# Kernel tuning notes

Hardware: AMD Instinct MI355X
Metric: run time of the kernel (lower is better)

The kernel has to match this reference:

```python
import jax, jax.numpy as jnp
import numpy as np

NEIGHBOR_RATE = 0.1  # neighbor_rate init arg
LEAKY_SLOPE = 0.2
NEG_INF = -1.0e9


def setup_inputs() -> dict:
    key = jax.random.key(0)
    k1, k2, k3, k4 = jax.random.split(key, 4)
    B, N, Din, H, hd = 4, 2048, 128, 4, 32  # output_dim = H*hd = 128
    h = jax.random.normal(k1, (B, N, Din), jnp.float32)
    adj = jax.random.uniform(k2, (B, N, N), jnp.float32)
    # stacked per-head params: W[k] in [Din, hd], a[k] in [2*hd]
    w_bound = 1.0 / np.sqrt(Din)
    a_bound = 1.0 / np.sqrt(2 * hd)
    W = jax.random.uniform(k3, (H, Din, hd), jnp.float32, -w_bound, w_bound)
    a = jax.random.uniform(k4, (H, 2 * hd), jnp.float32, -a_bound, a_bound)
    return {"h": h, "adj": adj, "W": W, "a": a}


def reference(h, adj, W, a):
    B, N, _ = h.shape
    H, _, hd = W.shape
    k = int(NEIGHBOR_RATE * N)  # num_neighbors
    # Wh: [B,H,N,hd]
    Wh = jnp.einsum('bnf,hfd->bhnd', h, W)
    # cat([Wh_i, Wh_j]) @ a  ==  Wh_i @ a[:hd] + Wh_j @ a[hd:] (broadcast trick)
    s_i = jnp.einsum('bhnd,hd->bhn', Wh, a[:, :hd])
    s_j = jnp.einsum('bhnd,hd->bhn', Wh, a[:, hd:])
    e = jax.nn.leaky_relu(s_i[..., :, None] + s_j[..., None, :], LEAKY_SLOPE)  # [B,H,N,N]
    # top-k mask along last (neighbor) axis, built by scatter like torch .scatter_
    _, idx = jax.lax.top_k(e, k)  # [B,H,N,k]
    row_mask = lambda i: jnp.zeros((N,), jnp.bool_).at[i].set(True)
    mask = jax.vmap(row_mask)(idx.reshape(-1, k)).reshape(e.shape)
    masked = jnp.where(mask, e, NEG_INF)
    attn = jax.nn.softmax(masked, axis=-1) * adj[:, None]  # [B,H,N,N]
    hp = jnp.einsum('bhnm,bhmd->bhnd', attn, Wh)
    # concat heads on feature dim -> [B,N,H*hd]
    return hp.transpose(0, 2, 1, 3).reshape(B, N, H * hd)
```

## Files before the change

kernel.cpp:

```cpp
#include <hip/hip_runtime.h>
#include <hip/hip_bf16.h>
#include <cmath>

#define BB 4
#define NN 2048
#define DIN 128
#define HH 4
#define HD 32
#define KSEL 204
#define BH (BB*HH)
#define KPAD 256
#define KST 264

typedef __attribute__((ext_vector_type(8))) short short8;
typedef __attribute__((ext_vector_type(4))) short short4v;
typedef __attribute__((ext_vector_type(4))) float float4v;

static __device__ inline short f2bf(float x) {
    __hip_bfloat16 b = __float2bfloat16(x);
    return __builtin_bit_cast(short, b);
}

__global__ __launch_bounds__(256) void s_kernel(const float* __restrict__ h,
                                                const float* __restrict__ W,
                                                const float* __restrict__ a,
                                                float* __restrict__ si, float* __restrict__ sj) {
    int bh = blockIdx.x >> 3, chunk = blockIdx.x & 7;
    int b = bh >> 2, hh = bh & 3;
    __shared__ float w1[128], w2[128];
    int t = threadIdx.x;
    {
        int f = t & 127, half = t >> 7;
        const float* Wp = W + (size_t)hh * (DIN * HD) + f * HD;
        const float* ap = a + hh * 64 + half * 32;
        float acc = 0.f;
#pragma unroll
        for (int d = 0; d < 32; ++d) acc += Wp[d] * ap[d];
        if (half == 0) w1[f] = acc; else w2[f] = acc;
    }
    __syncthreads();
    int n = chunk * 256 + t;
    const float4* hr = (const float4*)(h + ((size_t)b * NN + n) * DIN);
    float s1 = 0.f, s2 = 0.f;
#pragma unroll 8
    for (int q = 0; q < 32; ++q) {
        float4 x = hr[q];
        s1 += x.x * w1[q*4] + x.y * w1[q*4+1] + x.z * w1[q*4+2] + x.w * w1[q*4+3];
        s2 += x.x * w2[q*4] + x.y * w2[q*4+1] + x.z * w2[q*4+2] + x.w * w2[q*4+3];
    }
    int o = bh * NN + n;
    si[o] = s1; sj[o] = s2;
}

__global__ __launch_bounds__(1024) void select_kernel(
        const float* __restrict__ h, const float* __restrict__ W,
        const float* __restrict__ sj,
        int* __restrict__ idxsel, float* __restrict__ sjsel,
        float* __restrict__ sjmax, short* __restrict__ Whsel) {
    int bh = blockIdx.x;
    int b = bh >> 2, hh = bh & 3;
    int t = threadIdx.x, lane = t & 63, w = t >> 6;
    __shared__ float sv[NN];
    __shared__ short WT[32][136];
    __shared__ int hist16[16][256];
    __shared__ int binInfo[2];
    __shared__ int wtot[4];
    __shared__ int wtotg[16], wtote[16], woffg[16], woffe[16];
    __shared__ float wmax[16];
    __shared__ int idxLDS[KSEL];

    for (int e = t; e < 32 * 128; e += 1024) {
        int n = e >> 7, k = e & 127;
        WT[n][k] = f2bf(W[(size_t)hh * (DIN * HD) + k * HD + n]);
    }

    const float* s = sj + (size_t)bh * NN;
    int j0 = t * 2;
    float2 xx = *(const float2*)(s + j0);
    sv[j0] = xx.x; sv[j0 + 1] = xx.y;
    unsigned u0 = __builtin_bit_cast(unsigned, xx.x);
    unsigned u1 = __builtin_bit_cast(unsigned, xx.y);
    u0 = (u0 & 0x80000000u) ? ~u0 : (u0 | 0x80000000u);
    u1 = (u1 & 0x80000000u) ? ~u1 : (u1 | 0x80000000u);
    float lmax = fmaxf(xx.x, xx.y);
#pragma unroll
    for (int off = 32; off >= 1; off >>= 1) lmax = fmaxf(lmax, __shfl_xor(lmax, off));
    if (lane == 0) wmax[w] = lmax;
    __syncthreads();
    if (t == 0) {
        float m = wmax[0];
#pragma unroll
        for (int i = 1; i < 16; ++i) m = fmaxf(m, wmax[i]);
        sjmax[bh] = m;
    }

    unsigned prefix = 0;
    int need = KSEL;
#pragma unroll
    for (int shift = 24; shift >= 0; shift -= 8) {
        ((int*)hist16)[t] = 0; ((int*)hist16)[t + 1024] = 0;
        ((int*)hist16)[t + 2048] = 0; ((int*)hist16)[t + 3072] = 0;
        __syncthreads();
        unsigned hmask = (shift < 24) ? (0xFFFFFFFFu << (shift + 8)) : 0u;
        if (((u0 ^ prefix) & hmask) == 0) atomicAdd(&hist16[w][(u0 >> shift) & 255], 1);
        if (((u1 ^ prefix) & hmask) == 0) atomicAdd(&hist16[w][(u1 >> shift) & 255], 1);
        __syncthreads();
        int sc = 0, hv = 0, bb = 0;
        if (t < 256) {
            bb = 255 - t;
            hv = 0;
#pragma unroll
            for (int i = 0; i < 16; ++i) hv += hist16[i][bb];
            sc = hv;
#pragma unroll
            for (int off = 1; off < 64; off <<= 1) {
                int u = __shfl_up(sc, off);
                if (lane >= off) sc += u;
            }
            if (lane == 63) wtot[w] = sc;
        }
        __syncthreads();
        if (t < 256) {
            int woffset = 0;
#pragma unroll
            for (int i = 0; i < 4; ++i) woffset += (i < w) ? wtot[i] : 0;
            int incl = sc + woffset;
            int excl = incl - hv;
            if (incl >= need && excl < need) {
                binInfo[0] = bb;
                binInfo[1] = excl;
            }
        }
        __syncthreads();
        prefix |= ((unsigned)binInfo[0]) << shift;
        need -= binInfo[1];
        __syncthreads();
    }
    unsigned T = prefix;
    int n_gt = KSEL - need;

    int cg = (u0 > T ? 1 : 0) + (u1 > T ? 1 : 0);
    int ce = (u0 == T ? 1 : 0) + (u1 == T ? 1 : 0);
    int sg = cg, se = ce;
#pragma unroll
    for (int off = 1; off < 64; off <<= 1) {
        int ug = __shfl_up(sg, off), ue = __shfl_up(se, off);
        if (lane >= off) { sg += ug; se += ue; }
    }
    if (lane == 63) { wtotg[w] = sg; wtote[w] = se; }
    __syncthreads();
    if (t == 0) {
        int rg = 0, re = 0;
#pragma unroll
        for (int i = 0; i < 16; ++i) {
            woffg[i] = rg; rg += wtotg[i];
            woffe[i] = re; re += wtote[i];
        }
    }
    __syncthreads();
    int pg = woffg[w] + sg - cg;
    int te = woffe[w] + se - ce;
    {
        unsigned kk[2] = {u0, u1};
#pragma unroll
        for (int r = 0; r < 2; ++r) {
            int j = j0 + r;
            if (kk[r] > T) {
                idxsel[bh * KSEL + pg] = j;
                sjsel[bh * KSEL + pg] = sv[j];
                idxLDS[pg] = j;
                pg++;
            } else if (kk[r] == T) {
                if (te < need) {
                    int pos = n_gt + te;
                    idxsel[bh * KSEL + pos] = j;
                    sjsel[bh * KSEL + pos] = sv[j];
                    idxLDS[pos] = j;
                }
                te++;
            }
        }
    }
    __syncthreads();

    {
        int mr = lane & 15, quad = lane >> 4;
        int jjp = w * 16 + mr;
        bool valid = jjp < KSEL;
        const float* hrow = h + ((size_t)b * NN + (valid ? idxLDS[jjp] : 0)) * DIN + quad * 8;
        float4v acc0 = {0.f, 0.f, 0.f, 0.f};
        float4v acc1 = {0.f, 0.f, 0.f, 0.f};
#pragma unroll
        for (int ks = 0; ks < 4; ++ks) {
            short8 afr;
            if (valid) {
                float4 xa = *(const float4*)(hrow + ks * 32);
                float4 xb = *(const float4*)(hrow + ks * 32 + 4);
                afr[0] = f2bf(xa.x); afr[1] = f2bf(xa.y); afr[2] = f2bf(xa.z); afr[3] = f2bf(xa.w);
                afr[4] = f2bf(xb.x); afr[5] = f2bf(xb.y); afr[6] = f2bf(xb.z); afr[7] = f2bf(xb.w);
            } else {
                afr = (short8){0, 0, 0, 0, 0, 0, 0, 0};
            }
            short8 b0 = *(const short8*)&WT[mr][ks * 32 + quad * 8];
            short8 b1 = *(const short8*)&WT[16 + mr][ks * 32 + quad * 8];
            acc0 = __builtin_amdgcn_mfma_f32_16x16x32_bf16(afr, b0, acc0, 0, 0, 0);
            acc1 = __builtin_amdgcn_mfma_f32_16x16x32_bf16(afr, b1, acc1, 0, 0, 0);
        }
        short4v o0, o1;
#pragma unroll
        for (int r = 0; r < 4; ++r) { o0[r] = f2bf(acc0[r]); o1[r] = f2bf(acc1[r]); }
        size_t base = (size_t)bh * HD * KPAD;
        int jjs = w * 16 + quad * 4;
        *(short4v*)&Whsel[base + (size_t)mr * KPAD + jjs] = o0;
        *(short4v*)&Whsel[base + (size_t)(16 + mr) * KPAD + jjs] = o1;
    }
}

__global__ __launch_bounds__(256) void attn2_kernel(
        const float* __restrict__ adj, const float* __restrict__ si,
        const int* __restrict__ idxsel, const float* __restrict__ sjsel,
        const float* __restrict__ sjmax, const short* __restrict__ Whsel,
        float* __restrict__ out) {
    int b = blockIdx.x >> 7;
    int tile = blockIdx.x & 127;
    __shared__ float adjbuf[4][NN];
    __shared__ short PSb[HH][16][KST];
    __shared__ int   idxS[HH][KPAD];
    __shared__ float sjS[HH][KPAD];
    __shared__ float invZS[HH][16];
    __shared__ float smaxS[HH];
    int t = threadIdx.x, w = t >> 6, lane = t & 63;
    int mr = lane & 15, quad = lane >> 4;

    for (int e = t; e < HH * KPAD; e += 256) {
        int hh = e >> 8, jj = e & 255;
        bool v = jj < KSEL;
        idxS[hh][jj] = v ? idxsel[(b * HH + hh) * KSEL + jj] : 0;
        sjS[hh][jj]  = v ? sjsel[(b * HH + hh) * KSEL + jj] : -1e30f;
    }
    if (t < HH) smaxS[t] = sjmax[b * HH + t];

    short8 bfr[2][8];
    {
        const short* wp = Whsel + (size_t)((b * HH + w) * HD) * KPAD;
#pragma unroll
        for (int ni = 0; ni < 2; ++ni)
#pragma unroll
            for (int ks = 0; ks < 8; ++ks)
                bfr[ni][ks] = *(const short8*)(wp + (size_t)(ni * 16 + mr) * KPAD + ks * 32 + quad * 8);
    }

    int i0 = tile * 16;
    const float* adjb = adj + (size_t)b * NN * NN;
    {
        const float4* src = (const float4*)(adjb + (size_t)i0 * NN);
        float4* dst = (float4*)adjbuf;
#pragma unroll
        for (int q = 0; q < 8; ++q)
            dst[q * 256 + t] = src[q * 256 + t];
    }
    __syncthreads();

    int bh = b * HH + w;
    float smax = smaxS[w];
    for (int s = 0; s < 4; ++s) {
#pragma unroll
        for (int r = 0; r < 4; ++r) {
            int i_loc = s * 4 + r;
            int i = i0 + i_loc;
            float siv = si[(size_t)bh * NN + i];
            float m = siv + smax;
            m = (m >= 0.f) ? m : 0.2f * m;
            float z = 0.f;
            short* prow = &PSb[w][i_loc][0];
#pragma unroll
            for (int k = 0; k < 2; ++k) {
                int jj = k * 128 + lane * 2;
                int ja = idxS[w][jj], jb = idxS[w][jj + 1];
                float ava = adjbuf[r][ja], avb = adjbuf[r][jb];
                float ea = siv + sjS[w][jj];
                float eb = siv + sjS[w][jj + 1];
                ea = (ea >= 0.f) ? ea : 0.2f * ea;
                eb = (eb >= 0.f) ? eb : 0.2f * eb;
                float ca = __expf(ea - m);
                float cb = __expf(eb - m);
                z += ca + cb;
                short2 p;
                p.x = f2bf(ca * ava);
                p.y = f2bf(cb * avb);
                *(short2*)&prow[jj] = p;
            }
#pragma unroll
            for (int off = 32; off >= 1; off >>= 1) z += __shfl_xor(z, off);
            if (lane == 0) invZS[w][i_loc] = 1.0f / z;
        }
        if (s < 3) {
            __syncthreads();
            const float4* src = (const float4*)(adjb + (size_t)(i0 + (s + 1) * 4) * NN);
            float4* dst = (float4*)adjbuf;
#pragma unroll
            for (int q = 0; q < 8; ++q)
                dst[q * 256 + t] = src[q * 256 + t];
            __syncthreads();
        }
    }
#pragma unroll
    for (int ni = 0; ni < 2; ++ni) {
        float4v acc = {0.f, 0.f, 0.f, 0.f};
#pragma unroll
        for (int ks = 0; ks < 8; ++ks) {
            short8 afr = *(const short8*)&PSb[w][mr][ks * 32 + quad * 8];
            acc = __builtin_amdgcn_mfma_f32_16x16x32_bf16(afr, bfr[ni][ks], acc, 0, 0, 0);
        }
#pragma unroll
        for (int r = 0; r < 4; ++r) {
            int i_loc = quad * 4 + r;
            int d = ni * 16 + mr;
            out[((size_t)(b * NN + i0 + i_loc)) * (HH * HD) + w * HD + d] =
                acc[r] * invZS[w][i_loc];
        }
    }
}

extern "C" void kernel_launch(void* const* d_in, const int* in_sizes, int n_in,
                              void* d_out, int out_size, void* d_ws, size_t ws_size,
                              hipStream_t stream) {
    const float* h   = (const float*)d_in[0];
    const float* adj = (const float*)d_in[1];
    const float* W   = (const float*)d_in[2];
    const float* a   = (const float*)d_in[3];
    float* out = (float*)d_out;

    float* si     = (float*)d_ws;
    float* sj     = si + (size_t)BH * NN;
    float* sjsel  = sj + (size_t)BH * NN;
    float* sjmax  = sjsel + (size_t)BH * KSEL;
    int*   idxsel = (int*)(sjmax + 16);
    short* Whsel  = (short*)(idxsel + (size_t)BH * KSEL);

    s_kernel<<<BH * 8, 256, 0, stream>>>(h, W, a, si, sj);
    select_kernel<<<BH, 1024, 0, stream>>>(h, W, sj, idxsel, sjsel, sjmax, Whsel);
    attn2_kernel<<<BB * 128, 256, 0, stream>>>(adj, si, idxsel, sjsel, sjmax, Whsel, out);
}
```

Baseline: 127.9 us.

## Double-buffer adj rows via register prefetch and compute all heads per row in s_kernel

The attention kernel now stages adj in two-row chunks with a double-buffered LDS array, prefetching the next chunk into registers while the current rows are processed. This removes one barrier per step and hides global-load latency. The score kernel now has 4 threads share each h row and compute all 4 heads' dot products, reducing them with shuffles. This reads h once instead of once per head, but each block recomputes all heads' projected a-vectors.

```diff
diff --git a/kernel.cpp b/kernel.cpp
--- a/kernel.cpp
+++ b/kernel.cpp
@@ -25,31 +25,56 @@
                                                 const float* __restrict__ W,
                                                 const float* __restrict__ a,
                                                 float* __restrict__ si, float* __restrict__ sj) {
-    int bh = blockIdx.x >> 3, chunk = blockIdx.x & 7;
-    int b = bh >> 2, hh = bh & 3;
-    __shared__ float w1[128], w2[128];
+    __shared__ float w1L[HH][DIN], w2L[HH][DIN];
     int t = threadIdx.x;
-    {
-        int f = t & 127, half = t >> 7;
-        const float* Wp = W + (size_t)hh * (DIN * HD) + f * HD;
+    for (int e = t; e < 8 * DIN; e += 256) {
+        int f = e & 127, v = e >> 7;
+        int hh = v >> 1, half = v & 1;
+        const float* Wp = W + ((size_t)hh * DIN + f) * HD;
         const float* ap = a + hh * 64 + half * 32;
         float acc = 0.f;
 #pragma unroll
         for (int d = 0; d < 32; ++d) acc += Wp[d] * ap[d];
-        if (half == 0) w1[f] = acc; else w2[f] = acc;
-    }
-    __syncthreads();
-    int n = chunk * 256 + t;
-    const float4* hr = (const float4*)(h + ((size_t)b * NN + n) * DIN);
-    float s1 = 0.f, s2 = 0.f;
-#pragma unroll 8
-    for (int q = 0; q < 32; ++q) {
-        float4 x = hr[q];
-        s1 += x.x * w1[q*4] + x.y * w1[q*4+1] + x.z * w1[q*4+2] + x.w * w1[q*4+3];
-        s2 += x.x * w2[q*4] + x.y * w2[q*4+1] + x.z * w2[q*4+2] + x.w * w2[q*4+3];
-    }
-    int o = bh * NN + n;
-    si[o] = s1; sj[o] = s2;
+        if (half == 0) w1L[hh][f] = acc; else w2L[hh][f] = acc;
+    }
+    __syncthreads();
+
+    int gid = blockIdx.x * 256 + t;
+    int row = gid >> 2;
+    int q   = gid & 3;
+    int b = row >> 11, n = row & 2047;
+    const float* hr = h + (size_t)row * DIN;
+
+    float s1h0 = 0.f, s1h1 = 0.f, s1h2 = 0.f, s1h3 = 0.f;
+    float s2h0 = 0.f, s2h1 = 0.f, s2h2 = 0.f, s2h3 = 0.f;
+#pragma unroll
+    for (int i = 0; i < 8; ++i) {
+        int f = q * 4 + i * 16;
+        float4 x = *(const float4*)(hr + f);
+        const float* wa0 = &w1L[0][f]; const float* wb0 = &w2L[0][f];
+        const float* wa1 = &w1L[1][f]; const float* wb1 = &w2L[1][f];
+        const float* wa2 = &w1L[2][f]; const float* wb2 = &w2L[2][f];
+        const float* wa3 = &w1L[3][f]; const float* wb3 = &w2L[3][f];
+        s1h0 += x.x*wa0[0] + x.y*wa0[1] + x.z*wa0[2] + x.w*wa0[3];
+        s2h0 += x.x*wb0[0] + x.y*wb0[1] + x.z*wb0[2] + x.w*wb0[3];
+        s1h1 += x.x*wa1[0] + x.y*wa1[1] + x.z*wa1[2] + x.w*wa1[3];
+        s2h1 += x.x*wb1[0] + x.y*wb1[1] + x.z*wb1[2] + x.w*wb1[3];
+        s1h2 += x.x*wa2[0] + x.y*wa2[1] + x.z*wa2[2] + x.w*wa2[3];
+        s2h2 += x.x*wb2[0] + x.y*wb2[1] + x.z*wb2[2] + x.w*wb2[3];
+        s1h3 += x.x*wa3[0] + x.y*wa3[1] + x.z*wa3[2] + x.w*wa3[3];
+        s2h3 += x.x*wb3[0] + x.y*wb3[1] + x.z*wb3[2] + x.w*wb3[3];
+    }
+#pragma unroll
+    for (int off = 1; off <= 2; off <<= 1) {
+        s1h0 += __shfl_xor(s1h0, off); s2h0 += __shfl_xor(s2h0, off);
+        s1h1 += __shfl_xor(s1h1, off); s2h1 += __shfl_xor(s2h1, off);
+        s1h2 += __shfl_xor(s1h2, off); s2h2 += __shfl_xor(s2h2, off);
+        s1h3 += __shfl_xor(s1h3, off); s2h3 += __shfl_xor(s2h3, off);
+    }
+    float o1 = (q == 0) ? s1h0 : (q == 1) ? s1h1 : (q == 2) ? s1h2 : s1h3;
+    float o2 = (q == 0) ? s2h0 : (q == 1) ? s2h1 : (q == 2) ? s2h2 : s2h3;
+    size_t o = (size_t)(b * HH + q) * NN + n;
+    si[o] = o1; sj[o] = o2;
 }
 
 __global__ __launch_bounds__(1024) void select_kernel(
@@ -223,7 +248,7 @@
         float* __restrict__ out) {
     int b = blockIdx.x >> 7;
     int tile = blockIdx.x & 127;
-    __shared__ float adjbuf[4][NN];
+    __shared__ float adjbuf[2][2][NN];
     __shared__ short PSb[HH][16][KST];
     __shared__ int   idxS[HH][KPAD];
     __shared__ float sjS[HH][KPAD];
@@ -232,6 +257,16 @@
     int t = threadIdx.x, w = t >> 6, lane = t & 63;
     int mr = lane & 15, quad = lane >> 4;
 
+    int i0 = tile * 16;
+    const float* adjb = adj + (size_t)b * NN * NN + (size_t)i0 * NN;
+
+    float4 pre[4];
+    {
+        const float4* src = (const float4*)adjb;
+#pragma unroll
+        for (int q = 0; q < 4; ++q) pre[q] = src[q * 256 + t];
+    }
+
     for (int e = t; e < HH * KPAD; e += 256) {
         int hh = e >> 8, jj = e & 255;
         bool v = jj < KSEL;
@@ -250,25 +285,25 @@
                 bfr[ni][ks] = *(const short8*)(wp + (size_t)(ni * 16 + mr) * KPAD + ks * 32 + quad * 8);
     }
 
-    int i0 = tile * 16;
-    const float* adjb = adj + (size_t)b * NN * NN;
-    {
-        const float4* src = (const float4*)(adjb + (size_t)i0 * NN);
-        float4* dst = (float4*)adjbuf;
-#pragma unroll
-        for (int q = 0; q < 8; ++q)
-            dst[q * 256 + t] = src[q * 256 + t];
+    {
+        float4* dst = (float4*)(&adjbuf[0][0][0]);
+#pragma unroll
+        for (int q = 0; q < 4; ++q) dst[q * 256 + t] = pre[q];
     }
     __syncthreads();
 
     int bh = b * HH + w;
     float smax = smaxS[w];
-    for (int s = 0; s < 4; ++s) {
-#pragma unroll
-        for (int r = 0; r < 4; ++r) {
-            int i_loc = s * 4 + r;
-            int i = i0 + i_loc;
-            float siv = si[(size_t)bh * NN + i];
+    for (int s = 0; s < 8; ++s) {
+        if (s < 7) {
+            const float4* src = (const float4*)(adjb + (size_t)(s + 1) * 2 * NN);
+#pragma unroll
+            for (int q = 0; q < 4; ++q) pre[q] = src[q * 256 + t];
+        }
+#pragma unroll
+        for (int r = 0; r < 2; ++r) {
+            int i_loc = s * 2 + r;
+            float siv = si[(size_t)bh * NN + i0 + i_loc];
             float m = siv + smax;
             m = (m >= 0.f) ? m : 0.2f * m;
             float z = 0.f;
@@ -277,7 +312,7 @@
             for (int k = 0; k < 2; ++k) {
                 int jj = k * 128 + lane * 2;
                 int ja = idxS[w][jj], jb = idxS[w][jj + 1];
-                float ava = adjbuf[r][ja], avb = adjbuf[r][jb];
+                float ava = adjbuf[s & 1][r][ja], avb = adjbuf[s & 1][r][jb];
                 float ea = siv + sjS[w][jj];
                 float eb = siv + sjS[w][jj + 1];
                 ea = (ea >= 0.f) ? ea : 0.2f * ea;
@@ -294,15 +329,12 @@
             for (int off = 32; off >= 1; off >>= 1) z += __shfl_xor(z, off);
             if (lane == 0) invZS[w][i_loc] = 1.0f / z;
         }
-        if (s < 3) {
-            __syncthreads();
-            const float4* src = (const float4*)(adjb + (size_t)(i0 + (s + 1) * 4) * NN);
-            float4* dst = (float4*)adjbuf;
-#pragma unroll
-            for (int q = 0; q < 8; ++q)
-                dst[q * 256 + t] = src[q * 256 + t];
-            __syncthreads();
-        }
+        if (s < 7) {
+            float4* dst = (float4*)(&adjbuf[(s + 1) & 1][0][0]);
+#pragma unroll
+            for (int q = 0; q < 4; ++q) dst[q * 256 + t] = pre[q];
+        }
+        __syncthreads();
     }
 #pragma unroll
     for (int ni = 0; ni < 2; ++ni) {
@@ -338,7 +370,7 @@
     int*   idxsel = (int*)(sjmax + 16);
     short* Whsel  = (short*)(idxsel + (size_t)BH * KSEL);
 
-    s_kernel<<<BH * 8, 256, 0, stream>>>(h, W, a, si, sj);
+    s_kernel<<<128, 256, 0, stream>>>(h, W, a, si, sj);
     select_kernel<<<BH, 1024, 0, stream>>>(h, W, sj, idxsel, sjsel, sjmax, Whsel);
     attn2_kernel<<<BB * 128, 256, 0, stream>>>(adj, si, idxsel, sjsel, sjmax, Whsel, out);
 }
```

Result: slower. 135.1 us (+5.6%).
